# Performance work log

Hardware: AMD Instinct MI355X
Metric: run time of the kernel (lower is better)

Reference implementation:

```python
import jax, jax.numpy as jnp
import numpy as np

NUM_EXPERTS = 8
CAPACITY_FACTOR = 1.25


def setup_inputs() -> dict:
    key = jax.random.key(0)
    kx, kw = jax.random.split(key)
    x = jax.random.normal(kx, (8, 4096, 1024), dtype=jnp.float32)
    W = jax.random.normal(kw, (NUM_EXPERTS, 1024), dtype=jnp.float32) * (1.0 / np.sqrt(1024))
    return {"x": x, "W": W, "force_top_k": 2}


def reference(x, W, force_top_k):
    # Eval-mode router: no gate noise, no expert dropout (expert_dropout=0.0).
    B, S, D = x.shape
    num_tokens = B * S
    top_k = min(force_top_k, NUM_EXPERTS)

    x_flat = x.reshape(num_tokens, D)                       # [N, D]
    router_logits = x_flat @ W.T                            # [N, E]

    probs = jax.nn.softmax(router_logits, axis=-1)          # [N, E]
    dispatch_weights, expert_indices = jax.lax.top_k(probs, top_k)  # [N, k]

    total_capacity = int(num_tokens * top_k * CAPACITY_FACTOR)
    per_expert_capacity = max(1, total_capacity // NUM_EXPERTS)

    # one_hot(expert_indices).sum over k -> per-token expert mask [N, E]
    expert_mask = jax.nn.one_hot(expert_indices, NUM_EXPERTS, dtype=jnp.int32).sum(axis=1)
    tokens_per_expert = expert_mask.sum(axis=0).astype(jnp.float32)  # [E]
    capacity_mask = tokens_per_expert > per_expert_capacity
    num_dropped = capacity_mask.sum()

    avg_probs = probs.mean(axis=0)                          # [E]
    load_balance_loss = jnp.sum(
        tokens_per_expert / max(1, num_tokens) * avg_probs
    ) * NUM_EXPERTS

    log_probs = jax.nn.log_softmax(router_logits, axis=-1)
    entropy = -(probs * log_probs).sum(axis=-1).mean()
    target_entropy = jnp.log(jnp.float32(NUM_EXPERTS))
    router_entropy_loss = jnp.maximum(target_entropy - entropy, 0.0)

    expert_usage = tokens_per_expert / max(1, num_tokens)

    return (dispatch_weights, expert_indices, router_logits,
            load_balance_loss, router_entropy_loss, num_dropped, expert_usage)
```

## Files before the change

### kernel.cpp

```cpp
#include <hip/hip_runtime.h>

#define NTOK 32768
#define D 1024
#define NE 8
#define NWAVES 2048

template<int CTRL>
__device__ __forceinline__ float dpp_ror(float v) {
    return __int_as_float(
        __builtin_amdgcn_update_dpp(0, __float_as_int(v), CTRL, 0xf, 0xf, true));
}

__device__ __forceinline__ float row_reduce_add(float v) {
    v += dpp_ror<0x121>(v);
    v += dpp_ror<0x122>(v);
    v += dpp_ror<0x124>(v);
    v += dpp_ror<0x128>(v);
    return v;
}

__device__ __forceinline__ float wave_reduce_add(float v) {
    v = row_reduce_add(v);
    v += __shfl_xor(v, 16, 64);
    v += __shfl_xor(v, 32, 64);
    return v;
}

__device__ __forceinline__ float grp8_add(float v) {
    v += dpp_ror<0x121>(v);
    v += dpp_ror<0x122>(v);
    v += dpp_ror<0x124>(v);
    return v;
}
__device__ __forceinline__ float grp8_max(float v) {
    v = fmaxf(v, dpp_ror<0x121>(v));
    v = fmaxf(v, dpp_ror<0x122>(v));
    v = fmaxf(v, dpp_ror<0x124>(v));
    return v;
}
__device__ __forceinline__ float red_per_expert(float v) {
    v += dpp_ror<0x128>(v);
    v += __shfl_xor(v, 16, 64);
    v += __shfl_xor(v, 32, 64);
    return v;
}

__global__ __launch_bounds__(256, 2) void fused_kernel(
        const float* __restrict__ x, const float* __restrict__ W,
        float* __restrict__ logits, float* __restrict__ dw,
        float* __restrict__ eidx, float* __restrict__ ws) {
    const int lane = threadIdx.x & 63;
    const int wid  = (blockIdx.x * blockDim.x + threadIdx.x) >> 6;
    const int nw   = (gridDim.x * blockDim.x) >> 6;
    const int k    = lane & 7;

    float4 w[NE][4];
#pragma unroll
    for (int e = 0; e < NE; ++e)
#pragma unroll
        for (int c = 0; c < 4; ++c)
            w[e][c] = *(const float4*)(W + e * D + c * 256 + lane * 4);

    float p_acc = 0.f, c_acc = 0.f, ent_acc = 0.f;

    int t = wid;
    float4 xq[4];
    if (t < NTOK) {
        const float* xr = x + (size_t)t * D + lane * 4;
#pragma unroll
        for (int c = 0; c < 4; ++c) xq[c] = *(const float4*)(xr + c * 256);
    }

    while (t < NTOK) {
        const int tn = t + nw;
        float4 xn[4];
        if (tn < NTOK) {
            const float* xr = x + (size_t)tn * D + lane * 4;
#pragma unroll
            for (int c = 0; c < 4; ++c) xn[c] = *(const float4*)(xr + c * 256);
        }

        float acc[NE];
#pragma unroll
        for (int e = 0; e < NE; ++e) {
            float s = 0.f;
#pragma unroll
            for (int c = 0; c < 4; ++c) {
                s = fmaf(xq[c].x, w[e][c].x, s);
                s = fmaf(xq[c].y, w[e][c].y, s);
                s = fmaf(xq[c].z, w[e][c].z, s);
                s = fmaf(xq[c].w, w[e][c].w, s);
            }
            acc[e] = row_reduce_add(s);
        }

        float b0 = (k & 1) ? acc[1] : acc[0];
        float b1 = (k & 1) ? acc[3] : acc[2];
        float b2 = (k & 1) ? acc[5] : acc[4];
        float b3 = (k & 1) ? acc[7] : acc[6];
        float c0 = (k & 2) ? b1 : b0;
        float c1 = (k & 2) ? b3 : b2;
        float v  = (k & 4) ? c1 : c0;
        v += __shfl_xor(v, 16, 64);
        v += __shfl_xor(v, 32, 64);

        const float m    = grp8_max(v);
        const float pe   = __expf(v - m);
        const float S    = grp8_add(pe);
        const float p    = pe / S;
        const float logS = __logf(S);

        const float m1 = grp8_max(p);
        const unsigned long long b1m = __ballot(p == m1);
        const int e1 = __ffsll(b1m & 0xffull) - 1;
        const float cand = (k == e1) ? -1.0f : p;
        const float m2 = grp8_max(cand);
        const unsigned long long b2m = __ballot(cand == m2);
        const int e2 = __ffsll(b2m & 0xffull) - 1;

        if (lane < 8)       logits[t * 8 + lane] = v;
        if (lane == 0)      *(float2*)(dw   + t * 2) = make_float2(m1, m2);
        else if (lane == 1) *(float2*)(eidx + t * 2) = make_float2((float)e1, (float)e2);

        p_acc   += p;
        c_acc   += (float)((k == e1) + (k == e2));
        ent_acc += p * (v - m - logS);

        t = tn;
#pragma unroll
        for (int c = 0; c < 4; ++c) xq[c] = xn[c];
    }

    const float pr = red_per_expert(p_acc) * 0.125f;
    const float cr = red_per_expert(c_acc) * 0.125f;
    const float er = wave_reduce_add(ent_acc) * -0.125f;
    const float outv = (lane < 8) ? pr : ((lane < 16) ? cr : er);
    if (lane < 17) ws[wid * 17 + lane] = outv;
}

__global__ __launch_bounds__(256) void finalize_kernel(
        const float* __restrict__ ws, float* __restrict__ outs) {
    __shared__ float s_acc[17];
    const int tid = threadIdx.x;
    if (tid < 17) s_acc[tid] = 0.f;
    __syncthreads();

    float loc[17];
#pragma unroll
    for (int i = 0; i < 17; ++i) loc[i] = 0.f;
    for (int w = tid; w < NWAVES; w += 256) {
        const float* p = ws + w * 17;
#pragma unroll
        for (int i = 0; i < 17; ++i) loc[i] += p[i];
    }
#pragma unroll
    for (int i = 0; i < 17; ++i) {
        const float r = wave_reduce_add(loc[i]);
        if ((tid & 63) == 0) atomicAdd(&s_acc[i], r);
    }
    __syncthreads();

    if (tid == 0) {
        const float invN = 1.0f / 32768.0f;
        float lbl = 0.f, dropped = 0.f;
#pragma unroll
        for (int e = 0; e < 8; ++e) {
            const float cnt = s_acc[8 + e];
            lbl += (cnt * invN) * (s_acc[e] * invN);
            if (cnt > 10240.0f) dropped += 1.f;
            outs[3 + e] = cnt * invN;
        }
        outs[0] = lbl * 8.0f;
        const float ent = s_acc[16] * invN;
        outs[1] = fmaxf(2.0794415416798357f - ent, 0.0f);
        outs[2] = dropped;
    }
}

extern "C" void kernel_launch(void* const* d_in, const int* in_sizes, int n_in,
                              void* d_out, int out_size, void* d_ws, size_t ws_size,
                              hipStream_t stream) {
    const float* x = (const float*)d_in[0];
    const float* W = (const float*)d_in[1];
    float* out     = (float*)d_out;

    float* dw      = out;
    float* eidx    = out + 65536;
    float* logits  = out + 131072;
    float* scalars = out + 393216;
    float* ws      = (float*)d_ws;

    fused_kernel<<<512, 256, 0, stream>>>(x, W, logits, dw, eidx, ws);
    finalize_kernel<<<1, 256, 0, stream>>>(ws, scalars);
}
```

Measured before the change: 201.0 us.

## Process two adjacent tokens per wave iteration with paired prefetch and wider stores

Each wave now handles two consecutive tokens per loop iteration, interleaving their FMA chains, batching the DPP reductions, and writing logits, weights and indices for both tokens with wider stores. The prefetch loads the next pair of rows, so twice as much data is in flight per wave. The finalize kernel is widened from 256 to 1024 threads. Register pressure rises (two x buffers plus two prefetch buffers on top of 128 weight registers), which at launch bounds 256,2 could cause spills or lower occupancy on this memory-bound kernel.

Result: no change. 201.0 us (-0.0%).

```diff
diff --git a/kernel.cpp b/kernel.cpp
--- a/kernel.cpp
+++ b/kernel.cpp
@@ -4,6 +4,8 @@
 #define D 1024
 #define NE 8
 #define NWAVES 2048
+#define PAIR_STRIDE (2 * NWAVES)
+#define NPAIRIT (NTOK / PAIR_STRIDE)
 
 template<int CTRL>
 __device__ __forceinline__ float dpp_ror(float v) {
@@ -51,7 +53,6 @@
         float* __restrict__ eidx, float* __restrict__ ws) {
     const int lane = threadIdx.x & 63;
     const int wid  = (blockIdx.x * blockDim.x + threadIdx.x) >> 6;
-    const int nw   = (gridDim.x * blockDim.x) >> 6;
     const int k    = lane & 7;
 
     float4 w[NE][4];
@@ -63,72 +64,97 @@
 
     float p_acc = 0.f, c_acc = 0.f, ent_acc = 0.f;
 
-    int t = wid;
-    float4 xq[4];
-    if (t < NTOK) {
+    int t = wid * 2;
+    float4 xa[4], xb[4];
+    {
         const float* xr = x + (size_t)t * D + lane * 4;
 #pragma unroll
-        for (int c = 0; c < 4; ++c) xq[c] = *(const float4*)(xr + c * 256);
-    }
-
-    while (t < NTOK) {
-        const int tn = t + nw;
-        float4 xn[4];
-        if (tn < NTOK) {
-            const float* xr = x + (size_t)tn * D + lane * 4;
-#pragma unroll
-            for (int c = 0; c < 4; ++c) xn[c] = *(const float4*)(xr + c * 256);
-        }
-
-        float acc[NE];
+        for (int c = 0; c < 4; ++c) {
+            xa[c] = *(const float4*)(xr + c * 256);
+            xb[c] = *(const float4*)(xr + D + c * 256);
+        }
+    }
+
+    for (int it = 0; it < NPAIRIT; ++it) {
+        float4 na[4], nb[4];
+        if (it + 1 < NPAIRIT) {
+            const float* xr = x + (size_t)(t + PAIR_STRIDE) * D + lane * 4;
+#pragma unroll
+            for (int c = 0; c < 4; ++c) {
+                na[c] = *(const float4*)(xr + c * 256);
+                nb[c] = *(const float4*)(xr + D + c * 256);
+            }
+        }
+
+        float accA[NE], accB[NE];
 #pragma unroll
         for (int e = 0; e < NE; ++e) {
-            float s = 0.f;
+            float sa = 0.f, sb = 0.f;
 #pragma unroll
             for (int c = 0; c < 4; ++c) {
-                s = fmaf(xq[c].x, w[e][c].x, s);
-                s = fmaf(xq[c].y, w[e][c].y, s);
-                s = fmaf(xq[c].z, w[e][c].z, s);
-                s = fmaf(xq[c].w, w[e][c].w, s);
+                sa = fmaf(xa[c].x, w[e][c].x, sa);
+                sb = fmaf(xb[c].x, w[e][c].x, sb);
+                sa = fmaf(xa[c].y, w[e][c].y, sa);
+                sb = fmaf(xb[c].y, w[e][c].y, sb);
+                sa = fmaf(xa[c].z, w[e][c].z, sa);
+                sb = fmaf(xb[c].z, w[e][c].z, sb);
+                sa = fmaf(xa[c].w, w[e][c].w, sa);
+                sb = fmaf(xb[c].w, w[e][c].w, sb);
             }
-            acc[e] = row_reduce_add(s);
-        }
-
-        float b0 = (k & 1) ? acc[1] : acc[0];
-        float b1 = (k & 1) ? acc[3] : acc[2];
-        float b2 = (k & 1) ? acc[5] : acc[4];
-        float b3 = (k & 1) ? acc[7] : acc[6];
-        float c0 = (k & 2) ? b1 : b0;
-        float c1 = (k & 2) ? b3 : b2;
-        float v  = (k & 4) ? c1 : c0;
-        v += __shfl_xor(v, 16, 64);
-        v += __shfl_xor(v, 32, 64);
-
-        const float m    = grp8_max(v);
-        const float pe   = __expf(v - m);
-        const float S    = grp8_add(pe);
-        const float p    = pe / S;
-        const float logS = __logf(S);
-
-        const float m1 = grp8_max(p);
-        const unsigned long long b1m = __ballot(p == m1);
-        const int e1 = __ffsll(b1m & 0xffull) - 1;
-        const float cand = (k == e1) ? -1.0f : p;
-        const float m2 = grp8_max(cand);
-        const unsigned long long b2m = __ballot(cand == m2);
-        const int e2 = __ffsll(b2m & 0xffull) - 1;
-
-        if (lane < 8)       logits[t * 8 + lane] = v;
-        if (lane == 0)      *(float2*)(dw   + t * 2) = make_float2(m1, m2);
-        else if (lane == 1) *(float2*)(eidx + t * 2) = make_float2((float)e1, (float)e2);
-
-        p_acc   += p;
-        c_acc   += (float)((k == e1) + (k == e2));
-        ent_acc += p * (v - m - logS);
-
-        t = tn;
-#pragma unroll
-        for (int c = 0; c < 4; ++c) xq[c] = xn[c];
+            accA[e] = sa; accB[e] = sb;
+        }
+#pragma unroll
+        for (int e = 0; e < NE; ++e) {
+            accA[e] = row_reduce_add(accA[e]);
+            accB[e] = row_reduce_add(accB[e]);
+        }
+
+        float vv[2], w1[2], w2[2], ee1[2], ee2[2];
+#pragma unroll
+        for (int j = 0; j < 2; ++j) {
+            float a[NE];
+#pragma unroll
+            for (int e = 0; e < NE; ++e) a[e] = j ? accB[e] : accA[e];
+
+            float b0 = (k & 1) ? a[1] : a[0];
+            float b1 = (k & 1) ? a[3] : a[2];
+            float b2 = (k & 1) ? a[5] : a[4];
+            float b3 = (k & 1) ? a[7] : a[6];
+            float c0 = (k & 2) ? b1 : b0;
+            float c1 = (k & 2) ? b3 : b2;
+            float v  = (k & 4) ? c1 : c0;
+            v += __shfl_xor(v, 16, 64);
+            v += __shfl_xor(v, 32, 64);
+
+            const float m    = grp8_max(v);
+            const float pe   = __expf(v - m);
+            const float S    = grp8_add(pe);
+            const float p    = pe / S;
+            const float logS = __logf(S);
+
+            const float m1 = grp8_max(p);
+            const unsigned long long b1m = __ballot(p == m1);
+            const int e1 = __ffsll(b1m & 0xffull) - 1;
+            const float cand = (k == e1) ? -1.0f : p;
+            const float m2 = grp8_max(cand);
+            const unsigned long long b2m = __ballot(cand == m2);
+            const int e2 = __ffsll(b2m & 0xffull) - 1;
+
+            p_acc   += p;
+            c_acc   += (float)((k == e1) + (k == e2));
+            ent_acc += p * (v - m - logS);
+
+            vv[j] = v; w1[j] = m1; w2[j] = m2;
+            ee1[j] = (float)e1; ee2[j] = (float)e2;
+        }
+
+        if (lane < 16)      logits[t * 8 + lane] = (lane < 8) ? vv[0] : vv[1];
+        if (lane == 0)      *(float4*)(dw   + t * 2) = make_float4(w1[0],  w2[0],  w1[1],  w2[1]);
+        else if (lane == 1) *(float4*)(eidx + t * 2) = make_float4(ee1[0], ee2[0], ee1[1], ee2[1]);
+
+        t += PAIR_STRIDE;
+#pragma unroll
+        for (int c = 0; c < 4; ++c) { xa[c] = na[c]; xb[c] = nb[c]; }
     }
 
     const float pr = red_per_expert(p_acc) * 0.125f;
@@ -138,7 +164,7 @@
     if (lane < 17) ws[wid * 17 + lane] = outv;
 }
 
-__global__ __launch_bounds__(256) void finalize_kernel(
+__global__ __launch_bounds__(1024) void finalize_kernel(
         const float* __restrict__ ws, float* __restrict__ outs) {
     __shared__ float s_acc[17];
     const int tid = threadIdx.x;
@@ -148,7 +174,7 @@
     float loc[17];
 #pragma unroll
     for (int i = 0; i < 17; ++i) loc[i] = 0.f;
-    for (int w = tid; w < NWAVES; w += 256) {
+    for (int w = tid; w < NWAVES; w += 1024) {
         const float* p = ws + w * 17;
 #pragma unroll
         for (int i = 0; i < 17; ++i) loc[i] += p[i];
@@ -191,5 +217,5 @@
     float* ws      = (float*)d_ws;
 
     fused_kernel<<<512, 256, 0, stream>>>(x, W, logits, dw, eidx, ws);
-    finalize_kernel<<<1, 256, 0, stream>>>(ws, scalars);
-}
+    finalize_kernel<<<1, 1024, 0, stream>>>(ws, scalars);
+}
```
